# Optimization experiments

Hardware: AMD Instinct MI355X
Metric: run time of the kernel (lower is better)

## Reference

```python
import jax, jax.numpy as jnp
import numpy as np

C = 64; K = 3; KS = 7; A = 16
B, H, W = 4, 128, 128
EXTEND_SCOPE = 1.0
EPS = 1e-5

def _dct_mats(n):
    k = np.arange(n)[:, None]; m = np.arange(n)[None, :]
    D = 2.0 * np.cos(np.pi * (2 * m + 1) * k / (2.0 * n))  # torch_dct DCT-II, norm=None
    return jnp.asarray(D, jnp.float32), jnp.asarray(np.linalg.inv(D), jnp.float32)

_D, _Dinv = _dct_mats(K)

def _conv2d(x, w, b=None, stride=(1, 1), padding='SAME', groups=1):
    y = jax.lax.conv_general_dilated(x, w, stride, padding, feature_group_count=groups, dimension_numbers=('NCHW', 'OIHW', 'NCHW'))
    return y if b is None else y + b[None, :, None, None]

def _dwt(x):
    x1 = x[:, :, 0::2, 0::2] * 0.5; x2 = x[:, :, 1::2, 0::2] * 0.5
    x3 = x[:, :, 0::2, 1::2] * 0.5; x4 = x[:, :, 1::2, 1::2] * 0.5
    return (x1 + x2 + x3 + x4, -x1 + x2 - x3 + x4, -x1 - x2 + x3 + x4, x1 - x2 - x3 + x4)

def _iwt(LL, LH, HL, HH):
    a, b_, c, d = LL * 0.5, LH * 0.5, HL * 0.5, HH * 0.5
    n, ch, h, w = LL.shape
    out = jnp.zeros((n, ch, 2 * h, 2 * w), LL.dtype)
    out = out.at[:, :, 0::2, 0::2].set(a - b_ - c + d)
    out = out.at[:, :, 1::2, 0::2].set(a + b_ - c - d)
    out = out.at[:, :, 0::2, 1::2].set(a - b_ + c - d)
    out = out.at[:, :, 1::2, 1::2].set(a + b_ + c + d)
    return out

def _omni(x, fc_w, bn_g, bn_b, bn_m, bn_v, ch_w, ch_b, fl_w, fl_b, sp_w=None, sp_b=None):
    g = x.mean((2, 3))                                   # global avg pool -> [B,C]
    a = g @ fc_w.T
    a = jax.nn.relu((a - bn_m) * jax.lax.rsqrt(bn_v + EPS) * bn_g + bn_b)  # BN (eval)
    c_att = jax.nn.sigmoid(a @ ch_w.T + ch_b)
    f_att = jax.nn.sigmoid(a @ fl_w.T + fl_b)
    sp_att = None if sp_w is None else jax.nn.sigmoid(a @ sp_w.T + sp_b)
    return c_att, f_att, sp_att

def _forward(x, weight, ratio, o1_fc_w, o1_bn_g, o1_bn_b, o1_bn_m, o1_bn_v, o1_ch_w, o1_ch_b, o1_fl_w, o1_fl_b, o2_fc_w, o2_bn_g, o2_bn_b, o2_bn_m, o2_bn_v, o2_ch_w, o2_ch_b, o2_fl_w, o2_fl_b, o2_sp_w, o2_sp_b, off_w, off_b, obn_g, obn_b, obn_m, obn_v, ds_w, ds_b, gn_g, gn_b):
    b = x.shape[0]
    LL, LH, HL, HH = _dwt(x)
    c1, f1, _ = _omni(x, o1_fc_w, o1_bn_g, o1_bn_b, o1_bn_m, o1_bn_v, o1_ch_w, o1_ch_b, o1_fl_w, o1_fl_b)
    c2, f2, sp2 = _omni(x, o2_fc_w, o2_bn_g, o2_bn_b, o2_bn_m, o2_bn_v, o2_ch_w, o2_ch_b, o2_fl_w, o2_fl_b, o2_sp_w, o2_sp_b)
    # adaptive frequency-modulated dynamic kernels
    aw = jnp.broadcast_to(weight[None], (b,) + weight.shape)        # [B,Co,Ci,K,K]
    awm = aw.mean((-1, -2), keepdims=True)
    awr = aw - awm
    dctc = jnp.einsum('km,bojmn,ln->bojkl', _D, awr, _D)            # dct_2d
    dctc = dctc * (sp2.reshape(b, 1, 1, K, K) * 2.0)
    awr = jnp.einsum('km,bojmn,ln->bojkl', _Dinv, dctc, _Dinv)      # idct_2d
    aw = ratio * (awm * (c1[:, None, :, None, None] * 2) * (f1[:, :, None, None, None] * 2)) + (1.0 - ratio) * (awr * (c2[:, None, :, None, None] * 2) * (f2[:, :, None, None, None] * 2))
    # grouped conv (groups=b*C) then sum over c_in == depthwise conv with kernels summed over c_in (Cin==Cout)
    weff = aw.sum(axis=2)                                           # [B,C,K,K]
    h2, w2 = HH.shape[2], HH.shape[3]
    hh = _conv2d(HH.reshape(1, b * C, h2, w2), weff.reshape(b * C, 1, K, K), groups=b * C).reshape(b, C, h2, w2)
    out = _iwt(LL, LH, HL, hh) + x
    # ---- DSConv (dynamic snake conv, morph=0) ----
    off = _conv2d(out, off_w, off_b)
    off = (off - obn_m[None, :, None, None]) * jax.lax.rsqrt(obn_v + EPS)[None, :, None, None] * obn_g[None, :, None, None] + obn_b[None, :, None, None]
    y_off = jnp.tanh(off)[:, :KS]                                   # [B,KS,H,W]
    center = KS // 2
    low = jnp.flip(jnp.cumsum(jnp.flip(y_off[:, :center], 1), 1), 1)
    up = jnp.cumsum(y_off[:, center + 1:], 1)
    dy = jnp.concatenate([low, jnp.zeros_like(y_off[:, :1]), up], 1) * EXTEND_SCOPE
    hh_, ww_ = out.shape[2], out.shape[3]
    rows = jnp.clip(jnp.arange(hh_, dtype=x.dtype)[None, None, :, None] + dy, 0.0, hh_ - 1.0)
    cols = jnp.arange(ww_, dtype=x.dtype)[None, None, None, :] + (jnp.arange(KS, dtype=x.dtype) - center)[None, :, None, None]
    cols = jnp.clip(jnp.broadcast_to(cols, rows.shape), 0.0, ww_ - 1.0)
    r0 = jnp.floor(rows); c0 = jnp.floor(cols)
    wr = (rows - r0)[:, None]; wc = (cols - c0)[:, None]            # [B,1,KS,H,W]
    r0i = r0.astype(jnp.int32); c0i = c0.astype(jnp.int32)
    r1i = jnp.minimum(r0i + 1, hh_ - 1); c1i = jnp.minimum(c0i + 1, ww_ - 1)
    samp = jax.vmap(lambda img, ri, ci: img[:, ri, ci])             # [C,H,W],[KS,H,W] -> [C,KS,H,W]
    g00 = samp(out, r0i, c0i); g01 = samp(out, r0i, c1i)
    g10 = samp(out, r1i, c0i); g11 = samp(out, r1i, c1i)
    deform = (1 - wr) * (1 - wc) * g00 + (1 - wr) * wc * g01 + wr * (1 - wc) * g10 + wr * wc * g11
    deform = deform.transpose(0, 1, 3, 2, 4).reshape(b, C, hh_ * KS, ww_)
    y = _conv2d(deform, ds_w, ds_b, stride=(KS, 1), padding='VALID')  # [B,C,H,W]
    G = C // 4                                                       # GroupNorm(out//4)
    z = y.reshape(b, G, C // G, hh_, ww_)
    mu = z.mean((2, 3, 4), keepdims=True)
    var = ((z - mu) ** 2).mean((2, 3, 4), keepdims=True)
    y = ((z - mu) * jax.lax.rsqrt(var + EPS)).reshape(b, C, hh_, ww_)
    return jax.nn.relu(y * gn_g[None, :, None, None] + gn_b[None, :, None, None])

def setup_inputs() -> dict:
    key = jax.random.key(0)
    ks = jax.random.split(key, 12)
    def n(k, shape, s): return jax.random.normal(k, shape, jnp.float32) * s
    return dict(
        x=jax.random.normal(ks[0], (B, C, H, W), jnp.float32),
        weight=n(ks[1], (C, C, K, K), 0.1),
        ratio=jnp.asarray(0.5, jnp.float32),
        o1_fc_w=n(ks[2], (A, C), 0.2), o1_bn_g=jnp.ones((A,), jnp.float32), o1_bn_b=jnp.zeros((A,), jnp.float32),
        o1_bn_m=jnp.zeros((A,), jnp.float32), o1_bn_v=jnp.ones((A,), jnp.float32),
        o1_ch_w=n(ks[3], (C, A), 0.2), o1_ch_b=jnp.zeros((C,), jnp.float32),
        o1_fl_w=n(ks[4], (C, A), 0.2), o1_fl_b=jnp.zeros((C,), jnp.float32),
        o2_fc_w=n(ks[5], (A, C), 0.2), o2_bn_g=jnp.ones((A,), jnp.float32), o2_bn_b=jnp.zeros((A,), jnp.float32),
        o2_bn_m=jnp.zeros((A,), jnp.float32), o2_bn_v=jnp.ones((A,), jnp.float32),
        o2_ch_w=n(ks[6], (C, A), 0.2), o2_ch_b=jnp.zeros((C,), jnp.float32),
        o2_fl_w=n(ks[7], (C, A), 0.2), o2_fl_b=jnp.zeros((C,), jnp.float32),
        o2_sp_w=n(ks[8], (K * K, A), 0.2), o2_sp_b=jnp.zeros((K * K,), jnp.float32),
        off_w=n(ks[9], (2 * KS, C, 3, 3), 0.05), off_b=jnp.zeros((2 * KS,), jnp.float32),
        obn_g=jnp.ones((2 * KS,), jnp.float32), obn_b=jnp.zeros((2 * KS,), jnp.float32),
        obn_m=jnp.zeros((2 * KS,), jnp.float32), obn_v=jnp.ones((2 * KS,), jnp.float32),
        ds_w=n(ks[10], (C, C, KS, 1), 0.05), ds_b=jnp.zeros((C,), jnp.float32),
        gn_g=jnp.ones((C,), jnp.float32), gn_b=jnp.zeros((C,), jnp.float32),
    )

def reference(x, weight, ratio, o1_fc_w, o1_bn_g, o1_bn_b, o1_bn_m, o1_bn_v, o1_ch_w, o1_ch_b, o1_fl_w, o1_fl_b, o2_fc_w, o2_bn_g, o2_bn_b, o2_bn_m, o2_bn_v, o2_ch_w, o2_ch_b, o2_fl_w, o2_fl_b, o2_sp_w, o2_sp_b, off_w, off_b, obn_g, obn_b, obn_m, obn_v, ds_w, ds_b, gn_g, gn_b):
    return _forward(x, weight, ratio, o1_fc_w, o1_bn_g, o1_bn_b, o1_bn_m, o1_bn_v, o1_ch_w, o1_ch_b, o1_fl_w, o1_fl_b, o2_fc_w, o2_bn_g, o2_bn_b, o2_bn_m, o2_bn_v, o2_ch_w, o2_ch_b, o2_fl_w, o2_fl_b, o2_sp_w, o2_sp_b, off_w, off_b, obn_g, obn_b, obn_m, obn_v, ds_w, ds_b, gn_g, gn_b)
```

## Files before the change

### kernel.cpp

```cpp
#include <hip/hip_runtime.h>
#include <math.h>

#define BB 4
#define CC 64
#define HH_ 128
#define WW 128
#define HPW (HH_*WW)
#define KH 64
#define KW 64
#define KSZ 7
#define AA 16
#define EPSV 1e-5f
#define KTOT 448

typedef __attribute__((ext_vector_type(8))) short bf16x8;
typedef __attribute__((ext_vector_type(4))) float f32x4;
typedef unsigned short ushort_t;

__device__ __forceinline__ float sigm(float x){ return 1.0f/(1.0f+expf(-x)); }
__device__ __forceinline__ unsigned short f2bf(float f){
  unsigned u = __float_as_uint(f);
  return (unsigned short)((u + 0x7fffu + ((u>>16)&1u)) >> 16);
}

__global__ __launch_bounds__(512) void k_dwt0(const float* __restrict__ x,
  const float* __restrict__ dsw, const float* __restrict__ offw,
  float* __restrict__ HHb, float* __restrict__ partial,
  ushort_t* __restrict__ dsWbf, ushort_t* __restrict__ offAbf)
{
  int t = threadIdx.x; int wg = blockIdx.x;
  int idx = wg*512 + t;
  if(idx < CC*KTOT){
    int co = idx/KTOT; int K = idx%KTOT; int k = K>>6; int ci = K&63;
    dsWbf[idx] = f2bf(dsw[(size_t)(co*CC+ci)*KSZ + k]);
  } else {
    int j2 = idx - CC*KTOT;
    if(j2 < 18*16*32){
      int kl = j2&31; int co = (j2>>5)&15; int s = j2>>9;
      int tap = s>>1; int ci = (s&1)*32 + kl;
      float v = 0.f;
      if(co<KSZ) v = offw[((size_t)co*CC + ci)*9 + tap];
      offAbf[j2] = f2bf(v);
    }
  }
  int lane = t&63, wid = t>>6;
  int e0 = wg*2048 + t*4;
  int bc = e0>>12; int h2 = (e0>>6)&63; int w0 = e0&63;
  const float* xp = x + (size_t)bc*HPW;
  float4 a0 = *(const float4*)(xp + (2*h2)*WW + 2*w0);
  float4 a1 = *(const float4*)(xp + (2*h2)*WW + 2*w0 + 4);
  float4 b0 = *(const float4*)(xp + (2*h2+1)*WW + 2*w0);
  float4 b1 = *(const float4*)(xp + (2*h2+1)*WW + 2*w0 + 4);
  float4 hh;
  hh.x = 0.5f*(a0.x - b0.x - a0.y + b0.y);
  hh.y = 0.5f*(a0.z - b0.z - a0.w + b0.w);
  hh.z = 0.5f*(a1.x - b1.x - a1.y + b1.y);
  hh.w = 0.5f*(a1.z - b1.z - a1.w + b1.w);
  *(float4*)(HHb + e0) = hh;
  float s = a0.x+a0.y+a0.z+a0.w + a1.x+a1.y+a1.z+a1.w
          + b0.x+b0.y+b0.z+b0.w + b1.x+b1.y+b1.z+b1.w;
  for(int o=32;o>0;o>>=1) s += __shfl_down(s,o);
  __shared__ float ls[8];
  if(lane==0) ls[wid] = s;
  __syncthreads();
  if(t==0){
    float tot=0.f;
    #pragma unroll
    for(int k2=0;k2<8;k2++) tot += ls[k2];
    partial[wg] = tot;
  }
}

__global__ __launch_bounds__(64) void k_weff2(const float* __restrict__ partial,
  const float* __restrict__ w, const float* __restrict__ ratio_p,
  const float* __restrict__ o1fc, const float* __restrict__ o1g,const float* __restrict__ o1b,
  const float* __restrict__ o1m,const float* __restrict__ o1v,
  const float* __restrict__ o1cw,const float* __restrict__ o1cb,
  const float* __restrict__ o1fw,const float* __restrict__ o1fb,
  const float* __restrict__ o2fc, const float* __restrict__ o2g,const float* __restrict__ o2b,
  const float* __restrict__ o2m,const float* __restrict__ o2v,
  const float* __restrict__ o2cw,const float* __restrict__ o2cb,
  const float* __restrict__ o2fw,const float* __restrict__ o2fb,
  const float* __restrict__ spw,const float* __restrict__ spb,
  float* __restrict__ weff)
{
  int bo = blockIdx.x; int b = bo>>6, o = bo&63; int ci = threadIdx.x;
  int bc = b*CC+ci;
  float g_own = (partial[2*bc] + partial[2*bc+1]) * (1.0f/HPW);
  float d1=o1cb[ci], d2=o1fb[ci], d3=o2cb[ci], d4=o2fb[ci];
  float sspacc[9];
  #pragma unroll
  for(int e=0;e<9;e++) sspacc[e]=spb[e];
  for(int j=0;j<AA;j++){
    float p1 = g_own * o1fc[j*CC+ci];
    float p2 = g_own * o2fc[j*CC+ci];
    #pragma unroll
    for(int off=32;off>0;off>>=1){ p1+=__shfl_xor(p1,off); p2+=__shfl_xor(p2,off); }
    p1 = (p1-o1m[j])*rsqrtf(o1v[j]+EPSV)*o1g[j]+o1b[j]; p1=fmaxf(p1,0.f);
    p2 = (p2-o2m[j])*rsqrtf(o2v[j]+EPSV)*o2g[j]+o2b[j]; p2=fmaxf(p2,0.f);
    d1 += p1*o1cw[ci*AA+j]; d2 += p1*o1fw[ci*AA+j];
    d3 += p2*o2cw[ci*AA+j]; d4 += p2*o2fw[ci*AA+j];
    #pragma unroll
    for(int e=0;e<9;e++) sspacc[e] += p2*spw[e*AA+j];
  }
  float sc1v=sigm(d1), sc2v=sigm(d3);
  float sf1o=__shfl(sigm(d2),o), sf2o=__shfl(sigm(d4),o);
  const float* wp = w + (size_t)(o*CC+ci)*9;
  float w9[9]; float m=0.f;
  #pragma unroll
  for(int e=0;e<9;e++){ w9[e]=wp[e]; m+=w9[e]; }
  m *= (1.0f/9.0f);
  float S1 = m * sc1v;
  float M[9];
  #pragma unroll
  for(int e=0;e<9;e++) M[e] = (w9[e]-m)*sc2v;
  #pragma unroll
  for(int off=32; off>0; off>>=1){
    S1 += __shfl_xor(S1, off);
    #pragma unroll
    for(int e=0;e<9;e++) M[e] += __shfl_xor(M[e], off);
  }
  if(ci==0){
    const float Dm[3][3] = {{2.f,2.f,2.f},{1.7320508075688772f,0.f,-1.7320508075688772f},{1.f,-2.f,1.f}};
    const float Di[3][3] = {{0.16666666666666666f,0.28867513459481287f,0.16666666666666666f},
                            {0.16666666666666666f,0.f,-0.3333333333333333f},
                            {0.16666666666666666f,-0.28867513459481287f,0.16666666666666666f}};
    float U[3][3], T[3][3], V[3][3], R[3][3];
    for(int k=0;k<3;k++)for(int n=0;n<3;n++) U[k][n]=Dm[k][0]*M[0*3+n]+Dm[k][1]*M[1*3+n]+Dm[k][2]*M[2*3+n];
    for(int k=0;k<3;k++)for(int l=0;l<3;l++) T[k][l]=(U[k][0]*Dm[l][0]+U[k][1]*Dm[l][1]+U[k][2]*Dm[l][2])*2.0f*sigm(sspacc[k*3+l]);
    for(int k=0;k<3;k++)for(int n=0;n<3;n++) V[k][n]=Di[k][0]*T[0][n]+Di[k][1]*T[1][n]+Di[k][2]*T[2][n];
    for(int k=0;k<3;k++)for(int l=0;l<3;l++) R[k][l]=V[k][0]*Di[l][0]+V[k][1]*Di[l][1]+V[k][2]*Di[l][2];
    float rr = ratio_p[0];
    float base = rr*4.0f*sf1o*S1;
    float w2f = (1.0f-rr)*4.0f*sf2o;
    #pragma unroll
    for(int e=0;e<9;e++) weff[(size_t)bo*9+e] = base + w2f*R[e/3][e%3];
  }
}

__global__ __launch_bounds__(256) void k_iwtT(const float* __restrict__ HHb,
  const float* __restrict__ x, const float* __restrict__ weff,
  float* __restrict__ outT, ushort_t* __restrict__ outTbf)
{
  __shared__ __align__(16) char smem[25344 + 8320];
  float* hs  = (float*)smem;
  float* xt  = (float*)smem;
  float* d_s = (float*)(smem + 25344);
  int wg = blockIdx.x;
  int b = wg>>7; int idx7 = wg&127; int h2 = idx7>>1; int half = idx7&1;
  int t = threadIdx.x;
  for(int e=t; e<32*3*66; e+=256){
    int c_l = e/198; int rem = e - c_l*198; int r3 = rem/66; int wz = rem - r3*66;
    int r = h2 - 1 + r3; int w2 = wz - 1;
    int c = half*32 + c_l;
    float v = 0.f;
    if(r>=0 && r<KH && w2>=0 && w2<KW)
      v = HHb[((size_t)(b*CC+c))*(KH*KW) + r*KW + w2];
    hs[(c_l*3 + r3)*66 + wz] = v;
  }
  __syncthreads();
  {
    int c_l = t>>3, q = t&7;
    int c = half*32 + c_l;
    float wk[9];
    #pragma unroll
    for(int e=0;e<9;e++) wk[e] = weff[(size_t)(b*CC+c)*9+e];
    const float* hb = hs + c_l*198;
    #pragma unroll
    for(int j=0;j<8;j++){
      int w2 = q*8+j;
      float conv = 0.f;
      #pragma unroll
      for(int dh=0;dh<3;dh++){
        const float* hr = hb + dh*66 + w2;
        conv += wk[dh*3+0]*hr[0] + wk[dh*3+1]*hr[1] + wk[dh*3+2]*hr[2];
      }
      d_s[c_l*65+w2] = 0.5f*(conv - hb[1*66 + w2 + 1]);
    }
  }
  __syncthreads();
  #pragma unroll
  for(int r=0;r<2;r++){
    int h = 2*h2 + r;
    for(int e=t; e<32*WW; e+=256){
      int c_l=e>>7, w=e&127;
      xt[c_l*129+w] = x[((size_t)(b*CC+half*32+c_l)*HH_+h)*WW + w];
    }
    __syncthreads();
    float* dst = outT + ((size_t)(b*HH_+h))*WW*CC;
    ushort_t* dstb = outTbf + ((size_t)(b*HH_+h))*130*CC;
    for(int e=t; e<32*WW; e+=256){
      int w=e>>5, c_l=e&31; int c = half*32 + c_l;
      float dv = d_s[c_l*65+(w>>1)];
      float val = 2.f*xt[c_l*129+w] + (((h + w)&1) ? -dv : dv);
      dst[w*CC + c] = val;
      dstb[(w+1)*CC + c] = f2bf(val);
    }
    if(t<64){ int c_l=t&31; int side=t>>5; dstb[(size_t)side*129*CC + half*32 + c_l] = 0; }
    __syncthreads();
  }
}

__global__ __launch_bounds__(512) void k_dsfused(const float* __restrict__ outT,
  const ushort_t* __restrict__ outTbf, const ushort_t* __restrict__ dsWbf,
  const ushort_t* __restrict__ offAbf, const float* __restrict__ offb,
  const float* __restrict__ obg, const float* __restrict__ obb,
  const float* __restrict__ obm, const float* __restrict__ obv,
  const float* __restrict__ dsb, float* __restrict__ yout, float* __restrict__ pstats)
{
  __shared__ ushort_t S2a[2*8192];
  __shared__ int sb0[KSZ*128], sb1[KSZ*128];
  __shared__ float swr[KSZ*128];
  __shared__ float off_s[KSZ*128];
  __shared__ float dy_s[KSZ*128];
  int t = threadIdx.x;
  int wg = blockIdx.x; int sw = (wg&7)*64 + (wg>>3);
  int b = sw>>7, h = sw&127;
  int lane = t&63, wid = t>>6;
  int arow = lane&15, kgrp = lane>>4;
  {
    f32x4 acc = (f32x4){0.f,0.f,0.f,0.f};
    #pragma unroll
    for(int s=0;s<18;s++){
      int tap = s>>1, chalf = s&1;
      int r = tap/3, dwp = tap%3;
      int hr = h - 1 + r;
      if(hr<0 || hr>=HH_) continue;
      bf16x8 aF = *(const bf16x8*)(offAbf + (s*16+arow)*32 + kgrp*8);
      const ushort_t* base = outTbf + ((size_t)(b*HH_+hr))*130*CC + chalf*32 + kgrp*8;
      int wp = (wid<<4) + arow + dwp;
      bf16x8 bF = *(const bf16x8*)(base + (size_t)wp*CC);
      acc = __builtin_amdgcn_mfma_f32_16x16x32_bf16(aF, bF, acc, 0,0,0);
    }
    #pragma unroll
    for(int r=0;r<4;r++){
      int co = kgrp*4+r;
      if(co<KSZ) off_s[co*128 + (wid<<4) + arow] = acc[r];
    }
  }
  __syncthreads();
  if(t<128){
    int w = t;
    float y[KSZ];
    #pragma unroll
    for(int k=0;k<KSZ;k++){
      float sc = obg[k]*rsqrtf(obv[k]+EPSV);
      float sh = obb[k]-obm[k]*sc;
      y[k] = tanhf((off_s[k*128+w]+offb[k])*sc+sh);
    }
    dy_s[      w]=y[0]+y[1]+y[2]; dy_s[128+w]=y[1]+y[2]; dy_s[256+w]=y[2];
    dy_s[384+w]=0.f; dy_s[512+w]=y[4]; dy_s[640+w]=y[4]+y[5]; dy_s[768+w]=y[4]+y[5]+y[6];
  }
  __syncthreads();
  for(int e=t; e<KSZ*128; e+=512){
    int k = e>>7, w = e&127;
    float dv = dy_s[e];
    float r = fminf(fmaxf((float)h + dv, 0.f), 127.f);
    float rf = floorf(r); int r0=(int)rf; float wr=r-rf; int r1=min(r0+1,127);
    int c = min(max(w+k-3,0),127);
    sb0[k*128+w] = ((b*HH_+r0)*WW+c)*CC;
    sb1[k*128+w] = ((b*HH_+r1)*WW+c)*CC;
    swr[k*128+w] = wr;
  }
  __syncthreads();
  int cg2 = wid&3, wh = wid>>2;
  int rsub = lane>>4;
  int ciq  = (lane&15)<<2;
  {
    ushort_t* buf = S2a;
    #pragma unroll
    for(int i=0;i<4;i++){
      int p = (wid<<4) + i*4 + rsub;
      float4 v0 = *(const float4*)(outT + sb0[p] + ciq);
      float4 v1 = *(const float4*)(outT + sb1[p] + ciq);
      float wr = swr[p];
      unsigned lo = (unsigned)f2bf(v0.x + wr*(v1.x-v0.x)) | ((unsigned)f2bf(v0.y + wr*(v1.y-v0.y))<<16);
      unsigned hi = (unsigned)f2bf(v0.z + wr*(v1.z-v0.z)) | ((unsigned)f2bf(v0.w + wr*(v1.w-v0.w))<<16);
      int off = (p*128 + ciq*2) ^ ((p&7)<<4);
      *(uint2*)((char*)buf + off) = make_uint2(lo,hi);
    }
  }
  __syncthreads();
  f32x4 acc[4];
  #pragma unroll
  for(int nt=0;nt<4;nt++) acc[nt] = (f32x4){0.f,0.f,0.f,0.f};
  int bufs = 0;
  for(int k=0;k<KSZ;k++){
    if(k+1<KSZ){
      ushort_t* nb = S2a + (bufs^1)*8192;
      #pragma unroll
      for(int i=0;i<4;i++){
        int p = (wid<<4) + i*4 + rsub;
        int e = (k+1)*128 + p;
        float4 v0 = *(const float4*)(outT + sb0[e] + ciq);
        float4 v1 = *(const float4*)(outT + sb1[e] + ciq);
        float wr = swr[e];
        unsigned lo = (unsigned)f2bf(v0.x + wr*(v1.x-v0.x)) | ((unsigned)f2bf(v0.y + wr*(v1.y-v0.y))<<16);
        unsigned hi = (unsigned)f2bf(v0.z + wr*(v1.z-v0.z)) | ((unsigned)f2bf(v0.w + wr*(v1.w-v0.w))<<16);
        int off = (p*128 + ciq*2) ^ ((p&7)<<4);
        *(uint2*)((char*)nb + off) = make_uint2(lo,hi);
      }
    }
    const ushort_t* cb = S2a + bufs*8192;
    #pragma unroll
    for(int nt=0;nt<4;nt++){
      int pos = (wh<<6) + (nt<<4) + arow;
      int i0 = (pos<<6) + kgrp*8;
      int sz = (pos&7)<<3;
      bf16x8 b0 = *(const bf16x8*)(cb + (i0 ^ sz));
      bf16x8 b1 = *(const bf16x8*)(cb + ((i0+32) ^ sz));
      const ushort_t* Wp = dsWbf + (size_t)((cg2<<4)+arow)*KTOT + (k<<6) + kgrp*8;
      bf16x8 a0 = *(const bf16x8*)Wp;
      bf16x8 a1 = *(const bf16x8*)(Wp+32);
      acc[nt] = __builtin_amdgcn_mfma_f32_16x16x32_bf16(a0, b0, acc[nt], 0,0,0);
      acc[nt] = __builtin_amdgcn_mfma_f32_16x16x32_bf16(a1, b1, acc[nt], 0,0,0);
    }
    __syncthreads();
    bufs ^= 1;
  }
  float vs[4]={0.f,0.f,0.f,0.f}, vq[4]={0.f,0.f,0.f,0.f};
  #pragma unroll
  for(int r=0;r<4;r++){
    int co = (cg2<<4) + kgrp*4 + r;
    float bias = dsb[co];
    #pragma unroll
    for(int nt=0;nt<4;nt++){
      float y = acc[nt][r] + bias;
      int wcol = (wh<<6) + (nt<<4) + arow;
      yout[((size_t)(b*CC+co)*HH_ + h)*WW + wcol] = y;
      vs[r] += y; vq[r] += y*y;
    }
  }
  #pragma unroll
  for(int m=1;m<16;m<<=1){
    #pragma unroll
    for(int r=0;r<4;r++){ vs[r]+=__shfl_xor(vs[r],m); vq[r]+=__shfl_xor(vq[r],m); }
  }
  if(arow==0){
    #pragma unroll
    for(int r=0;r<4;r++){
      int co = (cg2<<4)+kgrp*4+r;
      int pi = (b*CC+co)*256 + h*2 + wh;
      pstats[pi] = vs[r];
      pstats[65536+pi] = vq[r];
    }
  }
}

__global__ __launch_bounds__(256) void k_gnfin2(const float* __restrict__ pstats,
                                                float* __restrict__ gstat){
  int bg = blockIdx.x; int b = bg>>4, g = bg&15; int t = threadIdx.x;
  float s=0.f, q=0.f;
  #pragma unroll
  for(int c4=0;c4<4;c4++){
    int base = (b*CC + g*4+c4)*256;
    s += pstats[base + t];
    q += pstats[65536 + base + t];
  }
  for(int o=32;o>0;o>>=1){ s+=__shfl_down(s,o); q+=__shfl_down(q,o); }
  __shared__ float ls[4], lq[4];
  if((t&63)==0){ ls[t>>6]=s; lq[t>>6]=q; }
  __syncthreads();
  if(t==0){
    float S=ls[0]+ls[1]+ls[2]+ls[3], Q=lq[0]+lq[1]+lq[2]+lq[3];
    float inv = 1.0f/(4.0f*HPW);
    float mu = S*inv; float var = Q*inv - mu*mu;
    gstat[bg*2]=mu; gstat[bg*2+1]=rsqrtf(var+EPSV);
  }
}

__global__ void k_gnapply(float* __restrict__ y, const float* __restrict__ gstat,
  const float* __restrict__ gg, const float* __restrict__ gb){
  int idx = blockIdx.x*256 + threadIdx.x;
  float4* p = (float4*)y;
  int bc = idx >> 12;
  int b = bc>>6, c = bc&63;
  int gi = b*16 + (c>>2);
  float mu = gstat[gi*2], rstd = gstat[gi*2+1];
  float sc = rstd*gg[c], sh = gb[c]-mu*sc;
  float4 v = p[idx];
  v.x = fmaxf(v.x*sc+sh, 0.f);
  v.y = fmaxf(v.y*sc+sh, 0.f);
  v.z = fmaxf(v.z*sc+sh, 0.f);
  v.w = fmaxf(v.w*sc+sh, 0.f);
  p[idx] = v;
}

extern "C" void kernel_launch(void* const* d_in, const int* in_sizes, int n_in,
                              void* d_out, int out_size, void* d_ws, size_t ws_size,
                              hipStream_t stream) {
  const float* x      = (const float*)d_in[0];
  const float* weight = (const float*)d_in[1];
  const float* ratio  = (const float*)d_in[2];
  const float* o1fc   = (const float*)d_in[3];
  const float* o1g    = (const float*)d_in[4];
  const float* o1b    = (const float*)d_in[5];
  const float* o1m    = (const float*)d_in[6];
  const float* o1v    = (const float*)d_in[7];
  const float* o1cw   = (const float*)d_in[8];
  const float* o1cb   = (const float*)d_in[9];
  const float* o1fw   = (const float*)d_in[10];
  const float* o1fb   = (const float*)d_in[11];
  const float* o2fc   = (const float*)d_in[12];
  const float* o2g    = (const float*)d_in[13];
  const float* o2b    = (const float*)d_in[14];
  const float* o2m    = (const float*)d_in[15];
  const float* o2v    = (const float*)d_in[16];
  const float* o2cw   = (const float*)d_in[17];
  const float* o2cb   = (const float*)d_in[18];
  const float* o2fw   = (const float*)d_in[19];
  const float* o2fb   = (const float*)d_in[20];
  const float* spw    = (const float*)d_in[21];
  const float* spb    = (const float*)d_in[22];
  const float* offw   = (const float*)d_in[23];
  const float* offb   = (const float*)d_in[24];
  const float* obg    = (const float*)d_in[25];
  const float* obb    = (const float*)d_in[26];
  const float* obm    = (const float*)d_in[27];
  const float* obv    = (const float*)d_in[28];
  const float* dsw    = (const float*)d_in[29];
  const float* dsb    = (const float*)d_in[30];
  const float* gng    = (const float*)d_in[31];
  const float* gnb    = (const float*)d_in[32];

  float* ws    = (float*)d_ws;
  float* HHb   = ws;
  float* partial = ws + 1048576;
  float* weff  = ws + 1049088;
  float* gstat = ws + 1051392;
  ushort_t* dsWbf  = (ushort_t*)(ws + 1051520);
  ushort_t* offAbf = (ushort_t*)(ws + 1065856);
  float* pstats= ws + 1070464;
  float* outT  = ws + 1201536;
  ushort_t* outTbf = (ushort_t*)(ws + 5395840);
  float* outb  = (float*)d_out;

  k_dwt0<<<512,512,0,stream>>>(x, dsw, offw, HHb, partial, dsWbf, offAbf);
  k_weff2<<<256,64,0,stream>>>(partial, weight, ratio,
    o1fc,o1g,o1b,o1m,o1v,o1cw,o1cb,o1fw,o1fb,
    o2fc,o2g,o2b,o2m,o2v,o2cw,o2cb,o2fw,o2fb,
    spw,spb, weff);
  k_iwtT<<<512,256,0,stream>>>(HHb, x, weff, outT, outTbf);
  k_dsfused<<<512,512,0,stream>>>(outT, outTbf, dsWbf, offAbf,
    offb, obg, obb, obm, obv, dsb, outb, pstats);
  k_gnfin2<<<64,256,0,stream>>>(pstats, gstat);
  k_gnapply<<<4096,256,0,stream>>>(outb, gstat, gng, gnb);
}
```

Baseline: 85.92 us.

## Drop fp32 outT buffer, sample bf16 padded copy, fuse GN finalize into apply

The iwt kernel no longer writes the fp32 channels-last output. The deformable sampling in k_dsfused now reads the bf16 padded buffer with 16-byte loads and interpolates in fp32 before repacking to bf16, which halves gather traffic and removes a 16MB write. The GroupNorm finalize kernel is folded into the apply kernel: each block recomputes its group's mean and rstd from the partial stats, saving one launch at the cost of redundant reductions. The sampled values now come from bf16-rounded inputs, so the result loses a little precision.

```diff
diff --git a/kernel.cpp b/kernel.cpp
--- a/kernel.cpp
+++ b/kernel.cpp
@@ -21,6 +21,9 @@
 __device__ __forceinline__ unsigned short f2bf(float f){
   unsigned u = __float_as_uint(f);
   return (unsigned short)((u + 0x7fffu + ((u>>16)&1u)) >> 16);
+}
+__device__ __forceinline__ float bf2f(unsigned short s){
+  return __uint_as_float(((unsigned)s)<<16);
 }
 
 __global__ __launch_bounds__(512) void k_dwt0(const float* __restrict__ x,
@@ -140,7 +143,7 @@
 
 __global__ __launch_bounds__(256) void k_iwtT(const float* __restrict__ HHb,
   const float* __restrict__ x, const float* __restrict__ weff,
-  float* __restrict__ outT, ushort_t* __restrict__ outTbf)
+  ushort_t* __restrict__ outTbf)
 {
   __shared__ __align__(16) char smem[25344 + 8320];
   float* hs  = (float*)smem;
@@ -187,13 +190,11 @@
       xt[c_l*129+w] = x[((size_t)(b*CC+half*32+c_l)*HH_+h)*WW + w];
     }
     __syncthreads();
-    float* dst = outT + ((size_t)(b*HH_+h))*WW*CC;
     ushort_t* dstb = outTbf + ((size_t)(b*HH_+h))*130*CC;
     for(int e=t; e<32*WW; e+=256){
       int w=e>>5, c_l=e&31; int c = half*32 + c_l;
       float dv = d_s[c_l*65+(w>>1)];
       float val = 2.f*xt[c_l*129+w] + (((h + w)&1) ? -dv : dv);
-      dst[w*CC + c] = val;
       dstb[(w+1)*CC + c] = f2bf(val);
     }
     if(t<64){ int c_l=t&31; int side=t>>5; dstb[(size_t)side*129*CC + half*32 + c_l] = 0; }
@@ -201,7 +202,7 @@
   }
 }
 
-__global__ __launch_bounds__(512) void k_dsfused(const float* __restrict__ outT,
+__global__ __launch_bounds__(512) void k_dsfused(
   const ushort_t* __restrict__ outTbf, const ushort_t* __restrict__ dsWbf,
   const ushort_t* __restrict__ offAbf, const float* __restrict__ offb,
   const float* __restrict__ obg, const float* __restrict__ obb,
@@ -258,49 +259,41 @@
     float r = fminf(fmaxf((float)h + dv, 0.f), 127.f);
     float rf = floorf(r); int r0=(int)rf; float wr=r-rf; int r1=min(r0+1,127);
     int c = min(max(w+k-3,0),127);
-    sb0[k*128+w] = ((b*HH_+r0)*WW+c)*CC;
-    sb1[k*128+w] = ((b*HH_+r1)*WW+c)*CC;
-    swr[k*128+w] = wr;
+    sb0[e] = ((b*HH_+r0)*130 + (c+1))*CC;
+    sb1[e] = ((b*HH_+r1)*130 + (c+1))*CC;
+    swr[e] = wr;
   }
   __syncthreads();
   int cg2 = wid&3, wh = wid>>2;
-  int rsub = lane>>4;
-  int ciq  = (lane&15)<<2;
-  {
-    ushort_t* buf = S2a;
-    #pragma unroll
-    for(int i=0;i<4;i++){
-      int p = (wid<<4) + i*4 + rsub;
-      float4 v0 = *(const float4*)(outT + sb0[p] + ciq);
-      float4 v1 = *(const float4*)(outT + sb1[p] + ciq);
-      float wr = swr[p];
-      unsigned lo = (unsigned)f2bf(v0.x + wr*(v1.x-v0.x)) | ((unsigned)f2bf(v0.y + wr*(v1.y-v0.y))<<16);
-      unsigned hi = (unsigned)f2bf(v0.z + wr*(v1.z-v0.z)) | ((unsigned)f2bf(v0.w + wr*(v1.w-v0.w))<<16);
-      int off = (p*128 + ciq*2) ^ ((p&7)<<4);
-      *(uint2*)((char*)buf + off) = make_uint2(lo,hi);
-    }
-  }
+  int psub = lane>>3;
+  int ci8  = (lane&7)<<3;
+  auto fill = [&](int k, ushort_t* buf){
+    #pragma unroll
+    for(int j=0;j<2;j++){
+      int p = (wid<<4) + j*8 + psub;
+      int e = k*128 + p;
+      bf16x8 r0 = *(const bf16x8*)(outTbf + sb0[e] + ci8);
+      bf16x8 r1 = *(const bf16x8*)(outTbf + sb1[e] + ci8);
+      float wr = swr[e];
+      unsigned o4[4];
+      #pragma unroll
+      for(int q=0;q<4;q++){
+        float a0 = bf2f((ushort_t)r0[2*q]),   b0v = bf2f((ushort_t)r1[2*q]);
+        float a1 = bf2f((ushort_t)r0[2*q+1]), b1v = bf2f((ushort_t)r1[2*q+1]);
+        o4[q] = (unsigned)f2bf(a0 + wr*(b0v-a0)) | ((unsigned)f2bf(a1 + wr*(b1v-a1))<<16);
+      }
+      int off = (p*128 + ci8*2) ^ ((p&7)<<4);
+      *(uint4*)((char*)buf + off) = make_uint4(o4[0],o4[1],o4[2],o4[3]);
+    }
+  };
+  fill(0, S2a);
   __syncthreads();
   f32x4 acc[4];
   #pragma unroll
   for(int nt=0;nt<4;nt++) acc[nt] = (f32x4){0.f,0.f,0.f,0.f};
   int bufs = 0;
   for(int k=0;k<KSZ;k++){
-    if(k+1<KSZ){
-      ushort_t* nb = S2a + (bufs^1)*8192;
-      #pragma unroll
-      for(int i=0;i<4;i++){
-        int p = (wid<<4) + i*4 + rsub;
-        int e = (k+1)*128 + p;
-        float4 v0 = *(const float4*)(outT + sb0[e] + ciq);
-        float4 v1 = *(const float4*)(outT + sb1[e] + ciq);
-        float wr = swr[e];
-        unsigned lo = (unsigned)f2bf(v0.x + wr*(v1.x-v0.x)) | ((unsigned)f2bf(v0.y + wr*(v1.y-v0.y))<<16);
-        unsigned hi = (unsigned)f2bf(v0.z + wr*(v1.z-v0.z)) | ((unsigned)f2bf(v0.w + wr*(v1.w-v0.w))<<16);
-        int off = (p*128 + ciq*2) ^ ((p&7)<<4);
-        *(uint2*)((char*)nb + off) = make_uint2(lo,hi);
-      }
-    }
+    if(k+1<KSZ) fill(k+1, S2a + (bufs^1)*8192);
     const ushort_t* cb = S2a + bufs*8192;
     #pragma unroll
     for(int nt=0;nt<4;nt++){
@@ -347,37 +340,34 @@
   }
 }
 
-__global__ __launch_bounds__(256) void k_gnfin2(const float* __restrict__ pstats,
-                                                float* __restrict__ gstat){
-  int bg = blockIdx.x; int b = bg>>4, g = bg&15; int t = threadIdx.x;
+__global__ __launch_bounds__(256) void k_gnapply(float* __restrict__ y,
+  const float* __restrict__ pstats, const float* __restrict__ gg, const float* __restrict__ gb){
+  int t = threadIdx.x;
+  int idx = blockIdx.x*256 + t;
+  int bc = idx >> 12;
+  int b = bc>>6, c = bc&63;
+  int g4 = c>>2;
   float s=0.f, q=0.f;
-  #pragma unroll
-  for(int c4=0;c4<4;c4++){
-    int base = (b*CC + g*4+c4)*256;
-    s += pstats[base + t];
-    q += pstats[65536 + base + t];
+  int base = (b*CC + g4*4)*256;
+  #pragma unroll
+  for(int i=0;i<4;i++){
+    s += pstats[base + i*256 + t];
+    q += pstats[65536 + base + i*256 + t];
   }
   for(int o=32;o>0;o>>=1){ s+=__shfl_down(s,o); q+=__shfl_down(q,o); }
-  __shared__ float ls[4], lq[4];
+  __shared__ float ls[4], lq[4], bcast[2];
   if((t&63)==0){ ls[t>>6]=s; lq[t>>6]=q; }
   __syncthreads();
   if(t==0){
     float S=ls[0]+ls[1]+ls[2]+ls[3], Q=lq[0]+lq[1]+lq[2]+lq[3];
     float inv = 1.0f/(4.0f*HPW);
     float mu = S*inv; float var = Q*inv - mu*mu;
-    gstat[bg*2]=mu; gstat[bg*2+1]=rsqrtf(var+EPSV);
-  }
-}
-
-__global__ void k_gnapply(float* __restrict__ y, const float* __restrict__ gstat,
-  const float* __restrict__ gg, const float* __restrict__ gb){
-  int idx = blockIdx.x*256 + threadIdx.x;
+    bcast[0]=mu; bcast[1]=rsqrtf(var+EPSV);
+  }
+  __syncthreads();
+  float mu = bcast[0], rstd = bcast[1];
+  float sc = rstd*gg[c], sh = gb[c]-mu*sc;
   float4* p = (float4*)y;
-  int bc = idx >> 12;
-  int b = bc>>6, c = bc&63;
-  int gi = b*16 + (c>>2);
-  float mu = gstat[gi*2], rstd = gstat[gi*2+1];
-  float sc = rstd*gg[c], sh = gb[c]-mu*sc;
   float4 v = p[idx];
   v.x = fmaxf(v.x*sc+sh, 0.f);
   v.y = fmaxf(v.y*sc+sh, 0.f);
@@ -427,12 +417,10 @@
   float* HHb   = ws;
   float* partial = ws + 1048576;
   float* weff  = ws + 1049088;
-  float* gstat = ws + 1051392;
-  ushort_t* dsWbf  = (ushort_t*)(ws + 1051520);
-  ushort_t* offAbf = (ushort_t*)(ws + 1065856);
-  float* pstats= ws + 1070464;
-  float* outT  = ws + 1201536;
-  ushort_t* outTbf = (ushort_t*)(ws + 5395840);
+  ushort_t* dsWbf  = (ushort_t*)(ws + 1051392);
+  ushort_t* offAbf = (ushort_t*)(ws + 1065728);
+  float* pstats= ws + 1070336;
+  ushort_t* outTbf = (ushort_t*)(ws + 1201408);
   float* outb  = (float*)d_out;
 
   k_dwt0<<<512,512,0,stream>>>(x, dsw, offw, HHb, partial, dsWbf, offAbf);
@@ -440,9 +428,8 @@
     o1fc,o1g,o1b,o1m,o1v,o1cw,o1cb,o1fw,o1fb,
     o2fc,o2g,o2b,o2m,o2v,o2cw,o2cb,o2fw,o2fb,
     spw,spb, weff);
-  k_iwtT<<<512,256,0,stream>>>(HHb, x, weff, outT, outTbf);
-  k_dsfused<<<512,512,0,stream>>>(outT, outTbf, dsWbf, offAbf,
+  k_iwtT<<<512,256,0,stream>>>(HHb, x, weff, outTbf);
+  k_dsfused<<<512,512,0,stream>>>(outTbf, dsWbf, offAbf,
     offb, obg, obb, obm, obv, dsb, outb, pstats);
-  k_gnfin2<<<64,256,0,stream>>>(pstats, gstat);
-  k_gnapply<<<4096,256,0,stream>>>(outb, gstat, gng, gnb);
-}
+  k_gnapply<<<4096,256,0,stream>>>(outb, pstats, gng, gnb);
+}
```

New measurement: 79.88 us. -7.0%, faster.
